# Performance work log

Measured on AMD Instinct MI355X. Metric: run time of the kernel, lower is better.

Reference implementation:

```python
import jax, jax.numpy as jnp
import numpy as np

N_BUCKET, EPB, K, TAU = 4, 4, 2, 1.0
C, H = 512, 1024
E = N_BUCKET * EPB
B, T = 2, 1024

def _l2norm(v):
    # matches F.normalize(dim=-1): v / max(||v||, 1e-12)
    return v / jnp.maximum(jnp.linalg.norm(v, axis=-1, keepdims=True), 1e-12)

def setup_inputs() -> dict:
    key = jax.random.key(0)
    ks = jax.random.split(key, 8)
    s = 1.0 / np.sqrt(C).astype(np.float32)
    sh = 1.0 / np.sqrt(H).astype(np.float32)
    return {
        "x": jax.random.normal(ks[0], (B, T, C), jnp.float32),
        "op_id": jax.random.randint(ks[1], (B, T), 0, N_BUCKET),
        "expert_key": jax.random.normal(ks[2], (N_BUCKET, EPB, C), jnp.float32) * s,
        "sW1": jax.random.normal(ks[3], (C, H), jnp.float32) * s,
        "sb1": jnp.zeros((H,), jnp.float32),
        "sW2": jax.random.normal(ks[4], (H, C), jnp.float32) * sh,
        "sb2": jnp.zeros((C,), jnp.float32),
        "eW1": jax.random.normal(ks[5], (E, C, H), jnp.float32) * s,
        "eb1": jnp.zeros((E, H), jnp.float32),
        "eW2": jax.random.normal(ks[6], (E, H, C), jnp.float32) * sh,
        "eb2": jnp.zeros((E, C), jnp.float32),
        "gate_logit": jnp.float32(-2.0),
    }

def reference(x, op_id, expert_key, sW1, sb1, sW2, sb2, eW1, eb1, eW2, eb2, gate_logit):
    Bb, Tt, Cc = x.shape
    # --- HierKVRouter ---
    bucket = jnp.clip(op_id, 0, N_BUCKET - 1)                 # (B,T)
    h_n = _l2norm(x)                                          # (B,T,C)
    keys = _l2norm(expert_key)                                # (nb,epb,C)
    keys_bt = keys[bucket]                                    # (B,T,epb,C) gather
    score = jnp.einsum('btc,btec->bte', h_n, keys_bt) / max(TAU, 1e-6)
    probs_local = jax.nn.softmax(score, axis=-1)              # (B,T,epb)
    topv, local = jax.lax.top_k(probs_local, K)               # (B,T,K)
    w = topv / (jnp.sum(topv, axis=-1, keepdims=True) + 1e-9) # combine weights
    gid = bucket[..., None] * EPB + local                     # (B,T,K) global ids
    # --- dispatch / expert MLP / combine ---
    flat_in = jnp.broadcast_to(x[:, :, None, :], (Bb, Tt, K, Cc)).reshape(-1, Cc)
    flat_gid = gid.reshape(-1)                                # (B*T*K,)
    flat_w = w.reshape(-1)                                    # (B*T*K,)
    out = jnp.zeros_like(flat_in)
    for e in range(E):  # fixed small expert count; masked dense = exact math of torch boolean-mask loop
        mask = (flat_gid == e)[:, None]
        h1 = jax.nn.relu(flat_in @ eW1[e] + eb1[e])
        oe = h1 @ eW2[e] + eb2[e]
        out = out + jnp.where(mask, oe * flat_w[:, None], 0.0)
    moe_out = out.reshape(Bb, Tt, K, Cc).sum(axis=2)          # (B,T,C)
    # --- shared dense FFN + gated combine ---
    dense = jax.nn.relu(x @ sW1 + sb1) @ sW2 + sb2
    y = dense + jax.nn.sigmoid(gate_logit) * moe_out
    return y
```

## Files before the change

### kernel.cpp

```cpp
#include <hip/hip_runtime.h>
#include <hip/hip_bf16.h>
#include <math.h>

#define C_DIM 512
#define H_DIM 1024
#define NTOK  2048
#define NSLOT 4096
#define NROWS 6144
#define MAXT128 64
#define MAXT64  112

typedef __attribute__((ext_vector_type(8))) short short8;
typedef __attribute__((ext_vector_type(4))) float floatx4;
typedef __attribute__((address_space(3))) void as3_void;
typedef const __attribute__((address_space(1))) void as1_cvoid;

__device__ __forceinline__ void gload_lds16(const void* g, void* l){
  __builtin_amdgcn_global_load_lds((as1_cvoid*)g, (as3_void*)l, 16, 0, 0);
}

__device__ __forceinline__ unsigned short f2b(float f){
  unsigned int u = __float_as_uint(f);
  unsigned int r = (u + 0x7FFFu + ((u >> 16) & 1u)) >> 16;
  return (unsigned short)r;
}

#define NB_CVT 1024
#define NB_RTR 512
#define NB_T1  2176
#define NB_T2  2176

__global__ __launch_bounds__(256) void k_prep(const float* __restrict__ x,
                                              const int* __restrict__ op_id,
                                              const float* __restrict__ ekey,
                                              const float* __restrict__ sW1,
                                              const float* __restrict__ sW2,
                                              const float* __restrict__ eW1,
                                              const float* __restrict__ eW2,
                                              unsigned short* __restrict__ Xb,
                                              unsigned short* __restrict__ sW1t,
                                              unsigned short* __restrict__ sW2t,
                                              unsigned short* __restrict__ eW1t,
                                              unsigned short* __restrict__ eW2t,
                                              int* __restrict__ gids,
                                              float* __restrict__ wv){
  __shared__ float tile[64 * 65];
  const int bid = blockIdx.x;
  const int tid = threadIdx.x;

  if (bid < NB_CVT){
    int i = bid * 256 + tid;
    float4 v = reinterpret_cast<const float4*>(x)[i];
    ushort4 o;
    o.x = f2b(v.x); o.y = f2b(v.y); o.z = f2b(v.z); o.w = f2b(v.w);
    reinterpret_cast<ushort4*>(Xb)[i] = o;
    return;
  }
  if (bid < NB_CVT + NB_RTR){
    int t = (bid - NB_CVT) * 4 + (tid >> 6);
    int lane = tid & 63;
    const float* xr = x + (size_t)t * C_DIM;
    float xs[8];
    float xn2 = 0.f;
    #pragma unroll
    for (int i = 0; i < 8; i++){ float v = xr[lane + 64*i]; xs[i] = v; xn2 += v*v; }
    #pragma unroll
    for (int o = 32; o; o >>= 1) xn2 += __shfl_xor(xn2, o, 64);
    int bucket = min(max(op_id[t], 0), 3);
    float xn = fmaxf(sqrtf(xn2), 1e-12f);
    float p[4];
    #pragma unroll
    for (int e = 0; e < 4; e++){
      const float* kr = ekey + ((size_t)bucket * 4 + e) * C_DIM;
      float dot = 0.f, kn2 = 0.f;
      #pragma unroll
      for (int i = 0; i < 8; i++){ float kv = kr[lane + 64*i]; dot += xs[i]*kv; kn2 += kv*kv; }
      #pragma unroll
      for (int o = 32; o; o >>= 1){ dot += __shfl_xor(dot, o, 64); kn2 += __shfl_xor(kn2, o, 64); }
      float kn = fmaxf(sqrtf(kn2), 1e-12f);
      p[e] = dot / (xn * kn);
    }
    float mx = fmaxf(fmaxf(p[0], p[1]), fmaxf(p[2], p[3]));
    float Z = 0.f;
    #pragma unroll
    for (int e = 0; e < 4; e++){ p[e] = expf(p[e] - mx); Z += p[e]; }
    #pragma unroll
    for (int e = 0; e < 4; e++) p[e] /= Z;
    int i0 = 0;
    #pragma unroll
    for (int e = 1; e < 4; e++) if (p[e] > p[i0]) i0 = e;
    int i1 = (i0 == 0) ? 1 : 0;
    #pragma unroll
    for (int e = 0; e < 4; e++) if (e != i0 && e != i1 && p[e] > p[i1]) i1 = e;
    float v0 = p[i0], v1 = p[i1];
    float wsum = v0 + v1 + 1e-9f;
    if (lane == 0){
      gids[2*t]   = bucket * 4 + i0;
      gids[2*t+1] = bucket * 4 + i1;
      wv[2*t]   = v0 / wsum;
      wv[2*t+1] = v1 / wsum;
    }
    return;
  }

  const float* in; unsigned short* out;
  int K, N, n0, k0;
  if (bid < NB_CVT + NB_RTR + NB_T1){
    int tb = bid - (NB_CVT + NB_RTR);
    int mat = tb >> 7, tl = tb & 127;
    K = C_DIM; N = H_DIM;
    in  = (mat < 16) ? eW1 + (size_t)mat * K * N : sW1;
    out = (mat < 16) ? eW1t + (size_t)mat * K * N : sW1t;
    n0 = (tl & 15) * 64; k0 = (tl >> 4) * 64;
  } else {
    int tb = bid - (NB_CVT + NB_RTR + NB_T1);
    int mat = tb >> 7, tl = tb & 127;
    K = H_DIM; N = C_DIM;
    in  = (mat < 16) ? eW2 + (size_t)mat * K * N : sW2;
    out = (mat < 16) ? eW2t + (size_t)mat * K * N : sW2t;
    n0 = (tl & 7) * 64; k0 = (tl >> 3) * 64;
  }
  {
    int tx = tid & 15, ty = tid >> 4;
    #pragma unroll
    for (int i = 0; i < 4; i++){
      int k = ty + 16 * i;
      float4 v = *reinterpret_cast<const float4*>(in + (size_t)(k0 + k) * N + n0 + tx * 4);
      tile[k * 65 + tx * 4 + 0] = v.x;
      tile[k * 65 + tx * 4 + 1] = v.y;
      tile[k * 65 + tx * 4 + 2] = v.z;
      tile[k * 65 + tx * 4 + 3] = v.w;
    }
    __syncthreads();
    #pragma unroll
    for (int i = 0; i < 4; i++){
      int n = ty + 16 * i;
      ushort4 o;
      o.x = f2b(tile[(4*tx + 0) * 65 + n]);
      o.y = f2b(tile[(4*tx + 1) * 65 + n]);
      o.z = f2b(tile[(4*tx + 2) * 65 + n]);
      o.w = f2b(tile[(4*tx + 3) * 65 + n]);
      *reinterpret_cast<ushort4*>(out + (size_t)(n0 + n) * K + k0 + 4 * tx) = o;
    }
  }
}

__global__ __launch_bounds__(256) void k_sort(const int* __restrict__ gids,
                                              int* __restrict__ inv,
                                              int* __restrict__ rowTok,
                                              int* __restrict__ tiles128,
                                              int* __restrict__ tiles64){
  __shared__ int hist[256][16];
  __shared__ int off[17];
  int t = threadIdx.x;
  int h[16];
  #pragma unroll
  for (int e = 0; e < 16; e++) h[e] = 0;
  int base = t * 16;
  for (int s = 0; s < 16; s++){ int g = gids[base + s]; h[g]++; }
  #pragma unroll
  for (int e = 0; e < 16; e++) hist[t][e] = h[e];
  __syncthreads();
  if (t < 16){
    int run = 0;
    for (int i = 0; i < 256; i++){ int v = hist[i][t]; hist[i][t] = run; run += v; }
    off[t + 1] = run;
  }
  __syncthreads();
  if (t == 0){ off[0] = 0; for (int e = 0; e < 16; e++) off[e+1] += off[e]; }
  __syncthreads();
  #pragma unroll
  for (int e = 0; e < 16; e++) h[e] = hist[t][e];
  for (int s = 0; s < 16; s++){
    int slot = base + s;
    int g = gids[slot];
    int pos = off[g] + h[g]; h[g]++;
    inv[slot] = pos;
    rowTok[NTOK + pos] = slot >> 1;
  }
  for (int r = t; r < NTOK; r += 256) rowTok[r] = r;
  __syncthreads();
  if (t == 0){
    int nt = 0;
    for (int r0 = 0; r0 < NTOK; r0 += 128){
      tiles128[nt*3] = r0; tiles128[nt*3+1] = 128; tiles128[nt*3+2] = 16; nt++;
    }
    for (int e = 0; e < 16; e++){
      int c = off[e+1] - off[e];
      for (int r0 = 0; r0 < c; r0 += 128){
        tiles128[nt*3] = NTOK + off[e] + r0;
        tiles128[nt*3+1] = min(128, c - r0);
        tiles128[nt*3+2] = e;
        nt++;
      }
    }
    for (int i = nt; i < MAXT128; i++){ tiles128[i*3] = 0; tiles128[i*3+1] = 0; tiles128[i*3+2] = 0; }
    nt = 0;
    for (int r0 = 0; r0 < NTOK; r0 += 64){
      tiles64[nt*3] = r0; tiles64[nt*3+1] = 64; tiles64[nt*3+2] = 16; nt++;
    }
    for (int e = 0; e < 16; e++){
      int c = off[e+1] - off[e];
      for (int r0 = 0; r0 < c; r0 += 64){
        tiles64[nt*3] = NTOK + off[e] + r0;
        tiles64[nt*3+1] = min(64, c - r0);
        tiles64[nt*3+2] = e;
        nt++;
      }
    }
    for (int i = nt; i < MAXT64; i++){ tiles64[i*3] = 0; tiles64[i*3+1] = 0; tiles64[i*3+2] = 0; }
  }
}

template<int BMT, int KDIM, int NDIM, bool RELU, bool OUTBF, bool GATHER>
__global__ __launch_bounds__(256) void k_gemm(const unsigned short* __restrict__ A,
                                              const unsigned short* __restrict__ BtE,
                                              const unsigned short* __restrict__ BtS,
                                              const float* __restrict__ biasE,
                                              const float* __restrict__ biasS,
                                              const int* __restrict__ rowTok,
                                              const int* __restrict__ tiles,
                                              unsigned short* __restrict__ outB,
                                              float* __restrict__ outF){
  const int tileId = blockIdx.x;
  const int rows = tiles[tileId*3+1];
  if (rows == 0) return;
  const int row0 = tiles[tileId*3];
  const int eid  = tiles[tileId*3+2];
  const unsigned short* Bt = (eid < 16) ? (BtE + (size_t)eid * NDIM * KDIM) : BtS;
  const float* bias = (eid < 16) ? (biasE + eid * NDIM) : biasS;
  const int n0 = blockIdx.y * 128;

  constexpr int MREP = BMT / 32;
  constexpr int AISS = BMT * 8 / 256;

  __shared__ __align__(16) unsigned short As[BMT * 64];
  __shared__ __align__(16) unsigned short Bs[128 * 64];

  const int tid = threadIdx.x;
  const int lane = tid & 63;
  const int wid = tid >> 6;
  const int wm = wid >> 1, wn = wid & 1;
  const int l15 = lane & 15, lhi = lane >> 4;

  int aRow[AISS], aOff[AISS];
  #pragma unroll
  for (int j = 0; j < AISS; j++){
    int c = j * 256 + tid;
    int i = c >> 3, op = c & 7;
    int o = op ^ (i & 7);
    int ie = min(i, rows - 1);
    aRow[j] = GATHER ? rowTok[row0 + ie] : (row0 + ie);
    aOff[j] = o * 8;
  }
  int bRow[4], bOff[4];
  #pragma unroll
  for (int j = 0; j < 4; j++){
    int c = j * 256 + tid;
    int i = c >> 3, op = c & 7;
    int o = op ^ (i & 7);
    bRow[j] = n0 + i;
    bOff[j] = o * 8;
  }

  floatx4 acc[MREP][4] = {};

  for (int kt = 0; kt < KDIM / 64; ++kt){
    #pragma unroll
    for (int j = 0; j < AISS; j++)
      gload_lds16(A + (size_t)aRow[j] * KDIM + kt * 64 + aOff[j],
                  (char*)As + (j * 256 + tid) * 16);
    #pragma unroll
    for (int j = 0; j < 4; j++)
      gload_lds16(Bt + (size_t)bRow[j] * KDIM + kt * 64 + bOff[j],
                  (char*)Bs + (j * 256 + tid) * 16);
    __syncthreads();
    #pragma unroll
    for (int kk = 0; kk < 2; ++kk){
      short8 a[MREP], b[4];
      #pragma unroll
      for (int m = 0; m < MREP; m++){
        int r = wm * (BMT/2) + m * 16 + l15;
        a[m] = *reinterpret_cast<const short8*>(
            (char*)As + r * 128 + ((kk * 64 + lhi * 16) ^ ((r & 7) << 4)));
      }
      #pragma unroll
      for (int n = 0; n < 4; n++){
        int r = wn * 64 + n * 16 + l15;
        b[n] = *reinterpret_cast<const short8*>(
            (char*)Bs + r * 128 + ((kk * 64 + lhi * 16) ^ ((r & 7) << 4)));
      }
      #pragma unroll
      for (int m = 0; m < MREP; m++)
        #pragma unroll
        for (int n = 0; n < 4; n++)
          acc[m][n] = __builtin_amdgcn_mfma_f32_16x16x32_bf16(a[m], b[n], acc[m][n], 0, 0, 0);
    }
    __syncthreads();
  }

  #pragma unroll
  for (int m = 0; m < MREP; m++){
    #pragma unroll
    for (int n = 0; n < 4; n++){
      int gcol = n0 + wn * 64 + n * 16 + l15;
      float bv = bias[gcol];
      #pragma unroll
      for (int q = 0; q < 4; q++){
        int ri = wm * (BMT/2) + m * 16 + lhi * 4 + q;
        if (ri < rows){
          float v = acc[m][n][q] + bv;
          if (RELU) v = fmaxf(v, 0.f);
          size_t o = (size_t)(row0 + ri) * NDIM + gcol;
          if (OUTBF) outB[o] = f2b(v); else outF[o] = v;
        }
      }
    }
  }
}

__global__ __launch_bounds__(256) void k_combine(const float* __restrict__ O,
                                                 const float* __restrict__ w,
                                                 const int* __restrict__ inv,
                                                 const float* __restrict__ gate,
                                                 float* __restrict__ y){
  int q = blockIdx.x * 256 + threadIdx.x;
  int t = q >> 7, c4 = q & 127;
  float sig = 1.f / (1.f + expf(-gate[0]));
  const float4* Of = reinterpret_cast<const float4*>(O);
  float4 d  = Of[(size_t)t * 128 + c4];
  int p0 = inv[2*t], p1 = inv[2*t+1];
  float w0 = w[2*t], w1 = w[2*t+1];
  float4 o0 = Of[(size_t)(NTOK + p0) * 128 + c4];
  float4 o1 = Of[(size_t)(NTOK + p1) * 128 + c4];
  float4 r;
  r.x = d.x + sig * (w0 * o0.x + w1 * o1.x);
  r.y = d.y + sig * (w0 * o0.y + w1 * o1.y);
  r.z = d.z + sig * (w0 * o0.z + w1 * o1.z);
  r.w = d.w + sig * (w0 * o0.w + w1 * o1.w);
  reinterpret_cast<float4*>(y)[q] = r;
}

extern "C" void kernel_launch(void* const* d_in, const int* in_sizes, int n_in,
                              void* d_out, int out_size, void* d_ws, size_t ws_size,
                              hipStream_t stream){
  const float* x    = (const float*)d_in[0];
  const int*   opid = (const int*)d_in[1];
  const float* ekey = (const float*)d_in[2];
  const float* sW1  = (const float*)d_in[3];
  const float* sb1  = (const float*)d_in[4];
  const float* sW2  = (const float*)d_in[5];
  const float* sb2  = (const float*)d_in[6];
  const float* eW1  = (const float*)d_in[7];
  const float* eb1  = (const float*)d_in[8];
  const float* eW2  = (const float*)d_in[9];
  const float* eb2  = (const float*)d_in[10];
  const float* gate = (const float*)d_in[11];
  float* y = (float*)d_out;

  char* ws = (char*)d_ws;
  size_t off = 0;
  auto alloc = [&](size_t bytes) -> char* {
    char* p = ws + off; off += (bytes + 255) & ~(size_t)255; return p;
  };
  unsigned short* Xb   = (unsigned short*)alloc((size_t)NTOK * C_DIM * 2);
  unsigned short* sW1t = (unsigned short*)alloc((size_t)H_DIM * C_DIM * 2);
  unsigned short* sW2t = (unsigned short*)alloc((size_t)C_DIM * H_DIM * 2);
  unsigned short* eW1t = (unsigned short*)alloc((size_t)16 * H_DIM * C_DIM * 2);
  unsigned short* eW2t = (unsigned short*)alloc((size_t)16 * C_DIM * H_DIM * 2);
  unsigned short* H1   = (unsigned short*)alloc((size_t)NROWS * H_DIM * 2);
  float* O      = (float*)alloc((size_t)NROWS * C_DIM * 4);
  float* wv     = (float*)alloc((size_t)NSLOT * 4);
  int*   gids   = (int*)alloc((size_t)NSLOT * 4);
  int*   inv    = (int*)alloc((size_t)NSLOT * 4);
  int*   rowTok = (int*)alloc((size_t)NROWS * 4);
  int*   tiles128 = (int*)alloc((size_t)MAXT128 * 3 * 4);
  int*   tiles64  = (int*)alloc((size_t)MAXT64 * 3 * 4);

  k_prep<<<NB_CVT + NB_RTR + NB_T1 + NB_T2, 256, 0, stream>>>(
      x, opid, ekey, sW1, sW2, eW1, eW2, Xb, sW1t, sW2t, eW1t, eW2t, gids, wv);
  k_sort<<<1, 256, 0, stream>>>(gids, inv, rowTok, tiles128, tiles64);
  k_gemm<128, C_DIM, H_DIM, true,  true,  true ><<<dim3(MAXT128, H_DIM/128), 256, 0, stream>>>(
      Xb, eW1t, sW1t, eb1, sb1, rowTok, tiles128, H1, nullptr);
  k_gemm<64,  H_DIM, C_DIM, false, false, false><<<dim3(MAXT64, C_DIM/128), 256, 0, stream>>>(
      H1, eW2t, sW2t, eb2, sb2, rowTok, tiles64, nullptr, O);
  k_combine<<<1024, 256, 0, stream>>>(O, wv, inv, gate, y);
}
```

Before: 82.30 us.

## Double-buffer GEMM LDS loads and fuse combine into second GEMM via atomics

The GEMM kernel now keeps two LDS buffers and issues the global-to-LDS loads for the next k-tile before computing the current one. It waits with explicit vmcnt counts and raw barriers so loads overlap the MFMA work. The separate combine kernel and the fp32 O buffer are removed: the second GEMM atomically adds weighted rows straight into y, with per-row weights (sigmoid gate times routing weight) precomputed in the sort kernel. This saves one launch and an O write plus read-back, but adds a memset of y, atomic traffic, and non-deterministic summation order.

Result: slower. 90.46 us (+9.9%).

```diff
diff --git a/kernel.cpp b/kernel.cpp
--- a/kernel.cpp
+++ b/kernel.cpp
@@ -146,13 +146,16 @@
 }
 
 __global__ __launch_bounds__(256) void k_sort(const int* __restrict__ gids,
-                                              int* __restrict__ inv,
+                                              const float* __restrict__ wv,
+                                              const float* __restrict__ gate,
                                               int* __restrict__ rowTok,
+                                              float* __restrict__ rowW,
                                               int* __restrict__ tiles128,
                                               int* __restrict__ tiles64){
   __shared__ int hist[256][16];
   __shared__ int off[17];
   int t = threadIdx.x;
+  float sig = 1.f / (1.f + expf(-gate[0]));
   int h[16];
   #pragma unroll
   for (int e = 0; e < 16; e++) h[e] = 0;
@@ -175,10 +178,10 @@
     int slot = base + s;
     int g = gids[slot];
     int pos = off[g] + h[g]; h[g]++;
-    inv[slot] = pos;
     rowTok[NTOK + pos] = slot >> 1;
-  }
-  for (int r = t; r < NTOK; r += 256) rowTok[r] = r;
+    rowW[NTOK + pos] = sig * wv[slot];
+  }
+  for (int r = t; r < NTOK; r += 256){ rowTok[r] = r; rowW[r] = 1.0f; }
   __syncthreads();
   if (t == 0){
     int nt = 0;
@@ -212,16 +215,17 @@
   }
 }
 
-template<int BMT, int KDIM, int NDIM, bool RELU, bool OUTBF, bool GATHER>
+template<int BMT, int KDIM, int NDIM, bool RELU, bool ATOMICY, bool GATHER>
 __global__ __launch_bounds__(256) void k_gemm(const unsigned short* __restrict__ A,
                                               const unsigned short* __restrict__ BtE,
                                               const unsigned short* __restrict__ BtS,
                                               const float* __restrict__ biasE,
                                               const float* __restrict__ biasS,
                                               const int* __restrict__ rowTok,
+                                              const float* __restrict__ rowW,
                                               const int* __restrict__ tiles,
                                               unsigned short* __restrict__ outB,
-                                              float* __restrict__ outF){
+                                              float* __restrict__ y){
   const int tileId = blockIdx.x;
   const int rows = tiles[tileId*3+1];
   if (rows == 0) return;
@@ -233,9 +237,10 @@
 
   constexpr int MREP = BMT / 32;
   constexpr int AISS = BMT * 8 / 256;
-
-  __shared__ __align__(16) unsigned short As[BMT * 64];
-  __shared__ __align__(16) unsigned short Bs[128 * 64];
+  constexpr int NLD  = AISS + 4;
+
+  __shared__ __align__(16) unsigned short As[2][BMT * 64];
+  __shared__ __align__(16) unsigned short Bs[2][128 * 64];
 
   const int tid = threadIdx.x;
   const int lane = tid & 63;
@@ -263,18 +268,32 @@
     bOff[j] = o * 8;
   }
 
-  floatx4 acc[MREP][4] = {};
-
-  for (int kt = 0; kt < KDIM / 64; ++kt){
+  auto STAGE = [&](int buf, int kt){
     #pragma unroll
     for (int j = 0; j < AISS; j++)
       gload_lds16(A + (size_t)aRow[j] * KDIM + kt * 64 + aOff[j],
-                  (char*)As + (j * 256 + tid) * 16);
+                  (char*)&As[buf][0] + (j * 256 + tid) * 16);
     #pragma unroll
     for (int j = 0; j < 4; j++)
       gload_lds16(Bt + (size_t)bRow[j] * KDIM + kt * 64 + bOff[j],
-                  (char*)Bs + (j * 256 + tid) * 16);
-    __syncthreads();
+                  (char*)&Bs[buf][0] + (j * 256 + tid) * 16);
+  };
+
+  floatx4 acc[MREP][4] = {};
+  constexpr int NT = KDIM / 64;
+
+  STAGE(0, 0);
+  for (int kt = 0; kt < NT; ++kt){
+    const int cur = kt & 1;
+    if (kt + 1 < NT){
+      STAGE(cur ^ 1, kt + 1);
+      if constexpr (NLD == 8) asm volatile("s_waitcnt vmcnt(8)" ::: "memory");
+      else                    asm volatile("s_waitcnt vmcnt(6)" ::: "memory");
+    } else {
+      asm volatile("s_waitcnt vmcnt(0)" ::: "memory");
+    }
+    __builtin_amdgcn_s_barrier();
+    asm volatile("" ::: "memory");
     #pragma unroll
     for (int kk = 0; kk < 2; ++kk){
       short8 a[MREP], b[4];
@@ -282,13 +301,13 @@
       for (int m = 0; m < MREP; m++){
         int r = wm * (BMT/2) + m * 16 + l15;
         a[m] = *reinterpret_cast<const short8*>(
-            (char*)As + r * 128 + ((kk * 64 + lhi * 16) ^ ((r & 7) << 4)));
+            (char*)&As[cur][0] + r * 128 + ((kk * 64 + lhi * 16) ^ ((r & 7) << 4)));
       }
       #pragma unroll
       for (int n = 0; n < 4; n++){
         int r = wn * 64 + n * 16 + l15;
         b[n] = *reinterpret_cast<const short8*>(
-            (char*)Bs + r * 128 + ((kk * 64 + lhi * 16) ^ ((r & 7) << 4)));
+            (char*)&Bs[cur][0] + r * 128 + ((kk * 64 + lhi * 16) ^ ((r & 7) << 4)));
       }
       #pragma unroll
       for (int m = 0; m < MREP; m++)
@@ -296,7 +315,8 @@
         for (int n = 0; n < 4; n++)
           acc[m][n] = __builtin_amdgcn_mfma_f32_16x16x32_bf16(a[m], b[n], acc[m][n], 0, 0, 0);
     }
-    __syncthreads();
+    asm volatile("" ::: "memory");
+    __builtin_amdgcn_s_barrier();
   }
 
   #pragma unroll
@@ -310,35 +330,17 @@
         int ri = wm * (BMT/2) + m * 16 + lhi * 4 + q;
         if (ri < rows){
           float v = acc[m][n][q] + bv;
-          if (RELU) v = fmaxf(v, 0.f);
-          size_t o = (size_t)(row0 + ri) * NDIM + gcol;
-          if (OUTBF) outB[o] = f2b(v); else outF[o] = v;
+          if constexpr (ATOMICY){
+            int tok = rowTok[row0 + ri];
+            atomicAdd(y + (size_t)tok * NDIM + gcol, v * rowW[row0 + ri]);
+          } else {
+            if (RELU) v = fmaxf(v, 0.f);
+            outB[(size_t)(row0 + ri) * NDIM + gcol] = f2b(v);
+          }
         }
       }
     }
   }
-}
-
-__global__ __launch_bounds__(256) void k_combine(const float* __restrict__ O,
-                                                 const float* __restrict__ w,
-                                                 const int* __restrict__ inv,
-                                                 const float* __restrict__ gate,
-                                                 float* __restrict__ y){
-  int q = blockIdx.x * 256 + threadIdx.x;
-  int t = q >> 7, c4 = q & 127;
-  float sig = 1.f / (1.f + expf(-gate[0]));
-  const float4* Of = reinterpret_cast<const float4*>(O);
-  float4 d  = Of[(size_t)t * 128 + c4];
-  int p0 = inv[2*t], p1 = inv[2*t+1];
-  float w0 = w[2*t], w1 = w[2*t+1];
-  float4 o0 = Of[(size_t)(NTOK + p0) * 128 + c4];
-  float4 o1 = Of[(size_t)(NTOK + p1) * 128 + c4];
-  float4 r;
-  r.x = d.x + sig * (w0 * o0.x + w1 * o1.x);
-  r.y = d.y + sig * (w0 * o0.y + w1 * o1.y);
-  r.z = d.z + sig * (w0 * o0.z + w1 * o1.z);
-  r.w = d.w + sig * (w0 * o0.w + w1 * o1.w);
-  reinterpret_cast<float4*>(y)[q] = r;
 }
 
 extern "C" void kernel_launch(void* const* d_in, const int* in_sizes, int n_in,
@@ -369,20 +371,19 @@
   unsigned short* eW1t = (unsigned short*)alloc((size_t)16 * H_DIM * C_DIM * 2);
   unsigned short* eW2t = (unsigned short*)alloc((size_t)16 * C_DIM * H_DIM * 2);
   unsigned short* H1   = (unsigned short*)alloc((size_t)NROWS * H_DIM * 2);
-  float* O      = (float*)alloc((size_t)NROWS * C_DIM * 4);
   float* wv     = (float*)alloc((size_t)NSLOT * 4);
   int*   gids   = (int*)alloc((size_t)NSLOT * 4);
-  int*   inv    = (int*)alloc((size_t)NSLOT * 4);
   int*   rowTok = (int*)alloc((size_t)NROWS * 4);
+  float* rowW   = (float*)alloc((size_t)NROWS * 4);
   int*   tiles128 = (int*)alloc((size_t)MAXT128 * 3 * 4);
   int*   tiles64  = (int*)alloc((size_t)MAXT64 * 3 * 4);
 
+  hipMemsetAsync(y, 0, (size_t)out_size * 4, stream);
   k_prep<<<NB_CVT + NB_RTR + NB_T1 + NB_T2, 256, 0, stream>>>(
       x, opid, ekey, sW1, sW2, eW1, eW2, Xb, sW1t, sW2t, eW1t, eW2t, gids, wv);
-  k_sort<<<1, 256, 0, stream>>>(gids, inv, rowTok, tiles128, tiles64);
-  k_gemm<128, C_DIM, H_DIM, true,  true,  true ><<<dim3(MAXT128, H_DIM/128), 256, 0, stream>>>(
-      Xb, eW1t, sW1t, eb1, sb1, rowTok, tiles128, H1, nullptr);
-  k_gemm<64,  H_DIM, C_DIM, false, false, false><<<dim3(MAXT64, C_DIM/128), 256, 0, stream>>>(
-      H1, eW2t, sW2t, eb2, sb2, rowTok, tiles64, nullptr, O);
-  k_combine<<<1024, 256, 0, stream>>>(O, wv, inv, gate, y);
-}
+  k_sort<<<1, 256, 0, stream>>>(gids, wv, gate, rowTok, rowW, tiles128, tiles64);
+  k_gemm<128, C_DIM, H_DIM, true,  false, true ><<<dim3(MAXT128, H_DIM/128), 256, 0, stream>>>(
+      Xb, eW1t, sW1t, eb1, sb1, rowTok, rowW, tiles128, H1, nullptr);
+  k_gemm<64,  H_DIM, C_DIM, false, true,  false><<<dim3(MAXT64, C_DIM/128), 256, 0, stream>>>(
+      H1, eW2t, sW2t, eb2, sb2, rowTok, rowW, tiles64, nullptr, y);
+}
```
